# Kernel optimization log

Hardware: AMD Instinct MI355X
Metric: run time of the kernel (lower is better)

The kernel has to match this reference:

```python
import jax, jax.numpy as jnp
import numpy as np

B, S1, S2, S3, I, O = 4, 64, 64, 64, 32, 32
MX, MZ = 16, 16
HID = O * 2  # factor=2 feedforward hidden


def setup_inputs() -> dict:
    key = jax.random.key(0)
    ks = jax.random.split(key, 5)
    x = jax.random.normal(ks[0], (B, S1, S2, S3, I), jnp.float32)
    # xavier-normal-ish scale for complex fourier weights stored as [...,2]
    sw = np.float32(np.sqrt(2.0 / (I + O)))
    wx = jax.random.normal(ks[1], (I, O, MX, 2), jnp.float32) * sw
    wz = jax.random.normal(ks[2], (I, O, MZ, 2), jnp.float32) * sw
    w1 = jax.random.normal(ks[3], (O, HID), jnp.float32) * np.float32(np.sqrt(1.0 / O))
    b1 = jnp.zeros((HID,), jnp.float32)
    w2 = jax.random.normal(ks[4], (HID, O), jnp.float32) * np.float32(np.sqrt(1.0 / HID))
    b2 = jnp.zeros((O,), jnp.float32)
    return {"x": x, "wx": wx, "wz": wz, "w1": w1, "b1": b1, "w2": w2, "b2": b2}


def _forward_fourier(x, wx, wz):
    # x: [b, i, s1, s2, s3]
    # z-axis branch
    cwz = wz[..., 0] + 1j * wz[..., 1]          # [i, o, mz] complex
    xfz = jnp.fft.rfft(x, axis=-1, norm='ortho')  # [b,i,s1,s2,S3//2+1]
    pz = jnp.einsum('bixyz,ioz->boxyz', xfz[..., :MZ], cwz)
    pz = jnp.pad(pz, ((0, 0), (0, 0), (0, 0), (0, 0), (0, S3 // 2 + 1 - MZ)))
    xz = jnp.fft.irfft(pz, n=S3, axis=-1, norm='ortho')
    # x-axis branch (note: modes_y branch contributes 0 in the source, xy=0.0)
    cwx = wx[..., 0] + 1j * wx[..., 1]          # [i, o, mx]
    xfx = jnp.fft.rfft(x, axis=2, norm='ortho')  # [b,i,S1//2+1,s2,s3]
    px = jnp.einsum('bixyz,iox->boxyz', xfx[:, :, :MX], cwx)
    px = jnp.pad(px, ((0, 0), (0, 0), (0, S1 // 2 + 1 - MX), (0, 0), (0, 0)))
    xx = jnp.fft.irfft(px, n=S1, axis=2, norm='ortho')
    return xx + xz


def reference(x, wx, wz, w1, b1, w2, b2):
    xt = jnp.transpose(x, (0, 4, 1, 2, 3))      # b i s1 s2 s3
    y = _forward_fourier(xt, wx, wz)
    y = jnp.transpose(y, (0, 2, 3, 4, 1))       # b s1 s2 s3 o
    # backcast FeedForward: Linear -> ReLU -> Linear (dropout=0, no norms)
    h = jax.nn.relu(y @ w1 + b1)
    b_out = h @ w2 + b2
    return b_out
```

## Files before the change

kernel.cpp:

```cpp
#include <hip/hip_runtime.h>

namespace {

typedef _Float16 half_t;
typedef half_t f16x2 __attribute__((ext_vector_type(2)));
typedef half_t f16x8 __attribute__((ext_vector_type(8)));
typedef float f32x4 __attribute__((ext_vector_type(4)));

constexpr size_t RSTR = 64 * 64 * 32;

constexpr int WS_TF = 0;
constexpr int WS_TI = 2048;
constexpr int WS_WZ = 4096;
constexpr int WS_WX = 69632;
constexpr int WS_W1 = 135168;
constexpr int WS_W2 = 137216;

__device__ __forceinline__ float f4get(const float4& v, int u) {
  return u == 0 ? v.x : (u == 1 ? v.y : (u == 2 ? v.z : v.w));
}

__device__ __forceinline__ f32x4 mfma16(f16x8 a, f16x8 b, f32x4 c) {
  return __builtin_amdgcn_mfma_f32_16x16x32_f16(a, b, c, 0, 0, 0);
}

__global__ __launch_bounds__(256) void kinit(const float* __restrict__ wx,
                                             const float* __restrict__ wz,
                                             const float* __restrict__ w1,
                                             const float* __restrict__ w2,
                                             half_t* __restrict__ wsh) {
  const int id = blockIdx.x * 256 + threadIdx.x;
  const int l = id & 63, r = l & 15, g = l >> 4;
  f16x8 frag;
  if (id < 256) {
    int fid = id >> 6, mt = fid >> 1, kt = fid & 1;
#pragma unroll
    for (int e = 0; e < 8; ++e) {
      int k = kt * 32 + 8 * g + e;
      int mc = mt * 16 + r, m = mc >> 1, p = mc & 1;
      float s, c;
      sincospif((float)(m * k) * (1.0f / 32.0f), &s, &c);
      frag[e] = (half_t)(0.125f * (p ? -s : c));
    }
    *(f16x8*)(wsh + WS_TF + (size_t)id * 8) = frag;
  } else if (id < 512) {
    int id2 = id - 256, mt = id2 >> 6;
#pragma unroll
    for (int e = 0; e < 8; ++e) {
      int zp = mt * 16 + r;
      int k = 8 * g + e, m = k >> 1, p = k & 1;
      float s, c;
      sincospif((float)(m * zp) * (1.0f / 32.0f), &s, &c);
      float sc = (m == 0) ? 0.125f : 0.25f;
      frag[e] = (half_t)(p ? -sc * s : sc * c);
    }
    *(f16x8*)(wsh + WS_TI + (size_t)id2 * 8) = frag;
  } else if (id < 16896) {
    int id2 = id - 512;
    const float* wsrc = wz;
    size_t off = WS_WZ;
    if (id2 >= 8192) { id2 -= 8192; wsrc = wx; off = WS_WX; }
    int fid = id2 >> 6, m = fid >> 3, kt = (fid >> 2) & 1, nt = fid & 3;
#pragma unroll
    for (int e = 0; e < 8; ++e) {
      int k = kt * 32 + 8 * g + e, i = k >> 1, p = k & 1;
      int n = nt * 16 + r, o = n >> 1, q = n & 1;
      int base = ((i * 32 + o) * 16 + m) * 2;
      float re = wsrc[base], im = wsrc[base + 1];
      frag[e] = (half_t)(q ? (p ? re : im) : (p ? -im : re));
    }
    *(f16x8*)(wsh + off + (size_t)id2 * 8) = frag;
  } else if (id < 17152) {
    int id2 = id - 16896, nt = id2 >> 6;
#pragma unroll
    for (int e = 0; e < 8; ++e) {
      int k = 8 * g + e, n = nt * 16 + r;
      frag[e] = (half_t)w1[k * 64 + n];
    }
    *(f16x8*)(wsh + WS_W1 + (size_t)id2 * 8) = frag;
  } else if (id < 17408) {
    int id2 = id - 17152, fid = id2 >> 6, kt = fid >> 1, nt = fid & 1;
#pragma unroll
    for (int e = 0; e < 8; ++e) {
      int k = kt * 32 + 8 * g + e, n = nt * 16 + r;
      frag[e] = (half_t)w2[k * 32 + n];
    }
    *(f16x8*)(wsh + WS_W2 + (size_t)id2 * 8) = frag;
  }
}

template <int BR>
__global__ __launch_bounds__(256) void kspec(const float* __restrict__ x,
                                             const half_t* __restrict__ wsh,
                                             const float* __restrict__ b1g,
                                             const float* __restrict__ b2g,
                                             float* __restrict__ outf) {
  __shared__ __align__(16) char smraw[49152];
  half_t* XB = (half_t*)smraw;
  half_t* FB = (half_t*)smraw;
  half_t* PB = (half_t*)(smraw + 32768);
  half_t* outh = (half_t*)outf;
  const int t = threadIdx.x, l = t & 63, w = t >> 6, r = l & 15, g = l >> 4;
  const f32x4 vzero = {0.f, 0.f, 0.f, 0.f};

  const int col0 = blockIdx.x * 8;
  size_t xbase = (size_t)col0 * 2048, zstr = 32, cstr = 2048;

  {
    int c = t >> 5, sub = t & 31;
    int i4 = (sub & 7) * 4, zq = sub >> 3;
    const float* xp = x + xbase + (size_t)c * cstr + i4;
#pragma unroll
    for (int zo = 0; zo < 2; ++zo) {
      int zb = zq * 16 + zo * 8;
      float4 v[8];
#pragma unroll
      for (int zz = 0; zz < 8; ++zz)
        v[zz] = *(const float4*)(xp + (size_t)(zb + zz) * zstr);
#pragma unroll
      for (int u = 0; u < 4; ++u) {
        f16x8 rowv;
#pragma unroll
        for (int zz = 0; zz < 8; ++zz) rowv[zz] = (half_t)f4get(v[zz], u);
        int rowi = c * 32 + i4 + u;
        int gr = (zb >> 3) ^ (rowi & 7);
        *(f16x8*)(XB + rowi * 64 + gr * 8) = rowv;
      }
    }
  }
  __syncthreads();

  f32x4 fa[2][4];
#pragma unroll
  for (int mt = 0; mt < 2; ++mt)
#pragma unroll
    for (int nt = 0; nt < 4; ++nt) fa[mt][nt] = vzero;
  {
    f16x8 Atf[2][2], Bx[4][2];
#pragma unroll
    for (int mt = 0; mt < 2; ++mt)
#pragma unroll
      for (int kt = 0; kt < 2; ++kt)
        Atf[mt][kt] = *(const f16x8*)(wsh + WS_TF + (size_t)((mt * 2 + kt) * 64 + l) * 8);
#pragma unroll
    for (int nt = 0; nt < 4; ++nt)
#pragma unroll
      for (int kt = 0; kt < 2; ++kt) {
        int rowi = w * 64 + nt * 16 + r;
        int gr = (kt * 4 + g) ^ (rowi & 7);
        Bx[nt][kt] = *(const f16x8*)(XB + rowi * 64 + gr * 8);
      }
#pragma unroll
    for (int kt = 0; kt < 2; ++kt)
#pragma unroll
      for (int nt = 0; nt < 4; ++nt)
#pragma unroll
        for (int mt = 0; mt < 2; ++mt)
          fa[mt][nt] = mfma16(Atf[mt][kt], Bx[nt][kt], fa[mt][nt]);
  }
  __syncthreads();

#pragma unroll
  for (int mt = 0; mt < 2; ++mt)
#pragma unroll
    for (int nt = 0; nt < 4; ++nt)
#pragma unroll
      for (int q = 0; q < 4; ++q) {
        int mc = mt * 16 + 4 * g + q, m = mc >> 1, p = mc & 1;
        int n = w * 64 + nt * 16 + r, c = n >> 5, i = n & 31;
        int k = 2 * i + p;
        FB[(m * 16 + c) * 64 + ((k >> 3) ^ (c & 7)) * 8 + (k & 7)] = (half_t)fa[mt][nt][q];
      }
  __syncthreads();

  const half_t* WF = wsh + WS_WZ;
#pragma unroll
  for (int j = 0; j < 4; ++j) {
    int m = w * 4 + j;
    f16x8 Af[2];
#pragma unroll
    for (int kt = 0; kt < 2; ++kt) {
      int gr = (kt * 4 + g) ^ (r & 7);
      Af[kt] = *(const f16x8*)(FB + (m * 16 + r) * 64 + gr * 8);
    }
    f32x4 pa[4];
#pragma unroll
    for (int nt = 0; nt < 4; ++nt) pa[nt] = vzero;
#pragma unroll
    for (int kt = 0; kt < 2; ++kt)
#pragma unroll
      for (int nt = 0; nt < 4; ++nt) {
        f16x8 Bw = *(const f16x8*)(WF + (size_t)((m * 8 + kt * 4 + nt) * 64 + l) * 8);
        pa[nt] = mfma16(Af[kt], Bw, pa[nt]);
      }
#pragma unroll
    for (int nt = 0; nt < 4; ++nt)
#pragma unroll
      for (int q = 0; q < 4; ++q) {
        int c = 4 * g + q;
        if (c < 8) {
          int n = nt * 16 + r, o = n >> 1, q2 = n & 1;
          int k = 2 * m + q2;
          PB[(c * 32 + o) * 32 + ((k >> 3) ^ (o & 3)) * 8 + (k & 7)] = (half_t)pa[nt][q];
        }
      }
  }
  __syncthreads();

  {
    f16x8 Ati[4];
#pragma unroll
    for (int mt = 0; mt < 4; ++mt)
      Ati[mt] = *(const f16x8*)(wsh + WS_TI + (size_t)(mt * 64 + l) * 8);
#pragma unroll
    for (int cc = 0; cc < 2; ++cc) {
      int c = w * 2 + cc;
      f16x8 Bp[2];
#pragma unroll
      for (int nt = 0; nt < 2; ++nt) {
        int o = nt * 16 + r;
        Bp[nt] = *(const f16x8*)(PB + (c * 32 + o) * 32 + (g ^ (o & 3)) * 8);
      }
      f32x4 ya[4][2];
#pragma unroll
      for (int mt = 0; mt < 4; ++mt)
#pragma unroll
        for (int nt = 0; nt < 2; ++nt) ya[mt][nt] = mfma16(Ati[mt], Bp[nt], vzero);
#pragma unroll
      for (int mt = 0; mt < 4; ++mt)
#pragma unroll
        for (int nt = 0; nt < 2; ++nt)
#pragma unroll
          for (int q = 0; q < 4; ++q) {
            int zp = mt * 16 + 4 * g + q, o = nt * 16 + r;
            outh[(size_t)(col0 + c) * 4096 + zp * 64 + o] = (half_t)ya[mt][nt][q];
          }
    }
  }
}

__global__ __launch_bounds__(256, 4) void kx4(const float* __restrict__ x,
                                              const half_t* __restrict__ wsh,
                                              const float* __restrict__ b1g,
                                              const float* __restrict__ b2g,
                                              float* __restrict__ outf) {
  __shared__ __align__(16) half_t smh[16384];
  half_t* XB = smh;
  half_t* FB = smh + 8192;
  half_t* PB = smh + 12288;
  half_t* YL = smh;
  half_t* HLa = smh + 8192;
  half_t* HLb = smh + 12288;
  half_t* outh = (half_t*)outf;
  const int t = threadIdx.x, l = t & 63, w = t >> 6, r = l & 15, g = l >> 4;
  const f32x4 vzero = {0.f, 0.f, 0.f, 0.f};

  const int d = blockIdx.x;
  const int pp = (d & 7) * 512 + (d >> 3);
  const int col0 = pp * 4;
  const int b = col0 >> 12, s2 = (col0 >> 6) & 63, s30 = col0 & 63;
  const size_t xbase = (size_t)b * 8388608 + (size_t)s2 * 2048 + (size_t)s30 * 32;

  {
    int sub = t & 31, zq = t >> 5;
    int c = sub >> 3, i4 = (sub & 7) * 4;
    const float* xp = x + xbase + (size_t)c * 32 + i4 + (size_t)(zq * 8) * RSTR;
    float4 v[8];
#pragma unroll
    for (int zz = 0; zz < 8; ++zz) v[zz] = *(const float4*)(xp + (size_t)zz * RSTR);
#pragma unroll
    for (int u = 0; u < 4; ++u) {
      f16x8 rowv;
#pragma unroll
      for (int zz = 0; zz < 8; ++zz) rowv[zz] = (half_t)f4get(v[zz], u);
      int rowi = c * 32 + i4 + u;
      int key = (rowi ^ (rowi >> 2)) & 7;
      *(f16x8*)(XB + rowi * 64 + (zq ^ key) * 8) = rowv;
    }
  }
  __syncthreads();

  f32x4 fa[2][2];
  {
    f16x8 Atf[2][2], Bx[2][2];
#pragma unroll
    for (int mt = 0; mt < 2; ++mt)
#pragma unroll
      for (int kt = 0; kt < 2; ++kt)
        Atf[mt][kt] = *(const f16x8*)(wsh + WS_TF + (size_t)((mt * 2 + kt) * 64 + l) * 8);
#pragma unroll
    for (int nt = 0; nt < 2; ++nt)
#pragma unroll
      for (int kt = 0; kt < 2; ++kt) {
        int rowi = w * 32 + nt * 16 + r;
        int key = (rowi ^ (rowi >> 2)) & 7;
        Bx[nt][kt] = *(const f16x8*)(XB + rowi * 64 + (((kt * 4 + g) ^ key)) * 8);
      }
#pragma unroll
    for (int mt = 0; mt < 2; ++mt)
#pragma unroll
      for (int nt = 0; nt < 2; ++nt) fa[mt][nt] = vzero;
#pragma unroll
    for (int kt = 0; kt < 2; ++kt)
#pragma unroll
      for (int nt = 0; nt < 2; ++nt)
#pragma unroll
        for (int mt = 0; mt < 2; ++mt)
          fa[mt][nt] = mfma16(Atf[mt][kt], Bx[nt][kt], fa[mt][nt]);
  }
#pragma unroll
  for (int mt = 0; mt < 2; ++mt)
#pragma unroll
    for (int nt = 0; nt < 2; ++nt)
#pragma unroll
      for (int pr = 0; pr < 2; ++pr) {
        int q = 2 * pr;
        int mc = mt * 16 + 4 * g + q, m = mc >> 1;
        int n = w * 32 + nt * 16 + r, c = n >> 5, i = n & 31;
        int k = 2 * i;
        f16x2 pairv = {(half_t)fa[mt][nt][q], (half_t)fa[mt][nt][q + 1]};
        *(f16x2*)(FB + (m * 4 + c) * 64 + (((k >> 3) ^ ((m + 2 * c) & 7))) * 8 + (k & 7)) =
            pairv;
      }
  __syncthreads();

#pragma unroll
  for (int j = 0; j < 4; ++j) {
    int m = w * 4 + j;
    int rsel = r & 3, keym = (m + 2 * rsel) & 7;
    f16x8 Af[2];
#pragma unroll
    for (int kt = 0; kt < 2; ++kt)
      Af[kt] = *(const f16x8*)(FB + (m * 4 + rsel) * 64 + (((kt * 4 + g) ^ keym)) * 8);
    f32x4 pa[4];
#pragma unroll
    for (int nt = 0; nt < 4; ++nt) pa[nt] = vzero;
#pragma unroll
    for (int kt = 0; kt < 2; ++kt)
#pragma unroll
      for (int nt = 0; nt < 4; ++nt) {
        f16x8 Bw = *(const f16x8*)(wsh + WS_WX + (size_t)((m * 8 + kt * 4 + nt) * 64 + l) * 8);
        pa[nt] = mfma16(Af[kt], Bw, pa[nt]);
      }
    if (g == 0) {
#pragma unroll
      for (int nt = 0; nt < 4; ++nt)
#pragma unroll
        for (int q = 0; q < 4; ++q) {
          int c = q;
          int n = nt * 16 + r, o = n >> 1, q2 = n & 1;
          int k = 2 * m + q2;
          PB[(c * 32 + o) * 32 + (((k >> 3) ^ (o & 3))) * 8 + (k & 7)] = (half_t)pa[nt][q];
        }
    }
  }
  __syncthreads();

  f16x8 Bp[2];
#pragma unroll
  for (int nt = 0; nt < 2; ++nt) {
    int o = nt * 16 + r;
    Bp[nt] = *(const f16x8*)(PB + (w * 32 + o) * 32 + ((g ^ (o & 3))) * 8);
  }
  f16x8 Ati[4];
#pragma unroll
  for (int mt = 0; mt < 4; ++mt)
    Ati[mt] = *(const f16x8*)(wsh + WS_TI + (size_t)(mt * 64 + l) * 8);
  f16x8 yzf[4];
#pragma unroll
  for (int rr = 0; rr < 4; ++rr) {
    int zp = rr * 16 + r;
    yzf[rr] = *(const f16x8*)(outh + ((size_t)(b * 64 + zp) * 64 + s2) * 4096 +
                              (size_t)(s30 + w) * 64 + 8 * g);
  }
  f16x8 W1F[4];
#pragma unroll
  for (int nt = 0; nt < 4; ++nt)
    W1F[nt] = *(const f16x8*)(wsh + WS_W1 + (size_t)(nt * 64 + l) * 8);
  float b1v[4];
#pragma unroll
  for (int nt = 0; nt < 4; ++nt) b1v[nt] = b1g[nt * 16 + r];

  half_t* YLw = YL + w * 2048;
  {
    f32x4 ya[4][2];
#pragma unroll
    for (int mt = 0; mt < 4; ++mt)
#pragma unroll
      for (int nt = 0; nt < 2; ++nt) ya[mt][nt] = mfma16(Ati[mt], Bp[nt], vzero);
#pragma unroll
    for (int mt = 0; mt < 4; ++mt)
#pragma unroll
      for (int nt = 0; nt < 2; ++nt)
#pragma unroll
        for (int q = 0; q < 4; ++q) {
          int zp = mt * 16 + 4 * g + q, o = nt * 16 + r;
          YLw[zp * 32 + (((o >> 3) ^ ((zp >> 2) & 3))) * 8 + (o & 7)] = (half_t)ya[mt][nt][q];
        }
  }
  f16x8 W2F[4];
#pragma unroll
  for (int f = 0; f < 4; ++f)
    W2F[f] = *(const f16x8*)(wsh + WS_W2 + (size_t)(f * 64 + l) * 8);
  float b2v[2];
#pragma unroll
  for (int nt = 0; nt < 2; ++nt) b2v[nt] = b2g[nt * 16 + r];

  half_t* HLwa = HLa + w * 1024;
  half_t* HLwb = HLb + w * 1024;
#pragma unroll
  for (int rr = 0; rr < 4; ++rr) {
    half_t* HLw = (rr & 1) ? HLwb : HLwa;
    int rowl = rr * 16 + r;
    f16x8 AY = *(const f16x8*)(YLw + rowl * 32 + ((g ^ ((rowl >> 2) & 3))) * 8);
    AY = AY + yzf[rr];
    f32x4 ha[4];
#pragma unroll
    for (int nt = 0; nt < 4; ++nt) ha[nt] = mfma16(AY, W1F[nt], vzero);
#pragma unroll
    for (int nt = 0; nt < 4; ++nt)
#pragma unroll
      for (int q = 0; q < 4; ++q) {
        int row4 = 4 * g + q, n = nt * 16 + r;
        float hv = fmaxf(ha[nt][q] + b1v[nt], 0.f);
        HLw[row4 * 64 + (((n >> 3) ^ g)) * 8 + (n & 7)] = (half_t)hv;
      }
    f16x8 AH[2];
#pragma unroll
    for (int kt = 0; kt < 2; ++kt)
      AH[kt] = *(const f16x8*)(HLw + r * 64 + (((kt * 4 + g) ^ (r >> 2))) * 8);
    f32x4 oa[2];
#pragma unroll
    for (int nt = 0; nt < 2; ++nt) oa[nt] = vzero;
#pragma unroll
    for (int kt = 0; kt < 2; ++kt)
#pragma unroll
      for (int nt = 0; nt < 2; ++nt) oa[nt] = mfma16(AH[kt], W2F[kt * 2 + nt], oa[nt]);
#pragma unroll
    for (int nt = 0; nt < 2; ++nt)
#pragma unroll
      for (int q = 0; q < 4; ++q) {
        int zp = rr * 16 + 4 * g + q, o = nt * 16 + r;
        outf[(size_t)b * 8388608 + (size_t)zp * RSTR + (size_t)s2 * 2048 +
             (size_t)(s30 + w) * 32 + o] = oa[nt][q] + b2v[nt];
      }
  }
}

}

extern "C" void kernel_launch(void* const* d_in, const int* in_sizes, int n_in,
                              void* d_out, int out_size, void* d_ws, size_t ws_size,
                              hipStream_t stream) {
  const float* x = (const float*)d_in[0];
  const float* wx = (const float*)d_in[1];
  const float* wz = (const float*)d_in[2];
  const float* w1 = (const float*)d_in[3];
  const float* b1 = (const float*)d_in[4];
  const float* w2 = (const float*)d_in[5];
  const float* b2 = (const float*)d_in[6];
  float* out = (float*)d_out;
  half_t* wsh = (half_t*)d_ws;

  hipLaunchKernelGGL(kinit, dim3(68), dim3(256), 0, stream, wx, wz, w1, w2, wsh);
  hipLaunchKernelGGL((kspec<0>), dim3(2048), dim3(256), 0, stream, x, wsh, b1, b2, out);
  hipLaunchKernelGGL(kx4, dim3(4096), dim3(256), 0, stream, x, wsh, b1, b2, out);
}
```

Baseline: 134.8 us.

## Load x fragments directly into registers and remap FFN rows across waves

Result: slower. 138.0 us (+2.4%).

```diff
diff --git a/kernel.cpp b/kernel.cpp
--- a/kernel.cpp
+++ b/kernel.cpp
@@ -244,13 +244,11 @@
                                               const float* __restrict__ b1g,
                                               const float* __restrict__ b2g,
                                               float* __restrict__ outf) {
-  __shared__ __align__(16) half_t smh[16384];
-  half_t* XB = smh;
-  half_t* FB = smh + 8192;
-  half_t* PB = smh + 12288;
+  __shared__ __align__(16) half_t smh[12288];
+  half_t* FB = smh;
+  half_t* PB = smh + 4096;
   half_t* YL = smh;
-  half_t* HLa = smh + 8192;
-  half_t* HLb = smh + 12288;
+  half_t* HL = smh + 8192;
   half_t* outh = (half_t*)outf;
   const int t = threadIdx.x, l = t & 63, w = t >> 6, r = l & 15, g = l >> 4;
   const f32x4 vzero = {0.f, 0.f, 0.f, 0.f};
@@ -261,41 +259,26 @@
   const int b = col0 >> 12, s2 = (col0 >> 6) & 63, s30 = col0 & 63;
   const size_t xbase = (size_t)b * 8388608 + (size_t)s2 * 2048 + (size_t)s30 * 32;
 
-  {
-    int sub = t & 31, zq = t >> 5;
-    int c = sub >> 3, i4 = (sub & 7) * 4;
-    const float* xp = x + xbase + (size_t)c * 32 + i4 + (size_t)(zq * 8) * RSTR;
-    float4 v[8];
-#pragma unroll
-    for (int zz = 0; zz < 8; ++zz) v[zz] = *(const float4*)(xp + (size_t)zz * RSTR);
-#pragma unroll
-    for (int u = 0; u < 4; ++u) {
-      f16x8 rowv;
-#pragma unroll
-      for (int zz = 0; zz < 8; ++zz) rowv[zz] = (half_t)f4get(v[zz], u);
-      int rowi = c * 32 + i4 + u;
-      int key = (rowi ^ (rowi >> 2)) & 7;
-      *(f16x8*)(XB + rowi * 64 + (zq ^ key) * 8) = rowv;
-    }
-  }
-  __syncthreads();
-
   f32x4 fa[2][2];
   {
-    f16x8 Atf[2][2], Bx[2][2];
+    f16x8 Bx[2][2];
+    const float* bp = x + xbase + (size_t)w * 32 + r;
+#pragma unroll
+    for (int nt = 0; nt < 2; ++nt)
+#pragma unroll
+      for (int kt = 0; kt < 2; ++kt) {
+        f16x8 fr;
+#pragma unroll
+        for (int e = 0; e < 8; ++e)
+          fr[e] = (half_t)bp[(size_t)(nt * 16) + (size_t)(kt * 32 + 8 * g + e) * RSTR];
+        Bx[nt][kt] = fr;
+      }
+    f16x8 Atf[2][2];
 #pragma unroll
     for (int mt = 0; mt < 2; ++mt)
 #pragma unroll
       for (int kt = 0; kt < 2; ++kt)
         Atf[mt][kt] = *(const f16x8*)(wsh + WS_TF + (size_t)((mt * 2 + kt) * 64 + l) * 8);
-#pragma unroll
-    for (int nt = 0; nt < 2; ++nt)
-#pragma unroll
-      for (int kt = 0; kt < 2; ++kt) {
-        int rowi = w * 32 + nt * 16 + r;
-        int key = (rowi ^ (rowi >> 2)) & 7;
-        Bx[nt][kt] = *(const f16x8*)(XB + rowi * 64 + (((kt * 4 + g) ^ key)) * 8);
-      }
 #pragma unroll
     for (int mt = 0; mt < 2; ++mt)
 #pragma unroll
@@ -362,6 +345,8 @@
     int o = nt * 16 + r;
     Bp[nt] = *(const f16x8*)(PB + (w * 32 + o) * 32 + ((g ^ (o & 3))) * 8);
   }
+  __syncthreads();
+
   f16x8 Ati[4];
 #pragma unroll
   for (int mt = 0; mt < 4; ++mt)
@@ -369,9 +354,8 @@
   f16x8 yzf[4];
 #pragma unroll
   for (int rr = 0; rr < 4; ++rr) {
-    int zp = rr * 16 + r;
-    yzf[rr] = *(const f16x8*)(outh + ((size_t)(b * 64 + zp) * 64 + s2) * 4096 +
-                              (size_t)(s30 + w) * 64 + 8 * g);
+    yzf[rr] = *(const f16x8*)(outh + ((size_t)(b * 64 + w * 16 + r) * 64 + s2) * 4096 +
+                              (size_t)(s30 + rr) * 64 + 8 * g);
   }
   f16x8 W1F[4];
 #pragma unroll
@@ -380,8 +364,6 @@
   float b1v[4];
 #pragma unroll
   for (int nt = 0; nt < 4; ++nt) b1v[nt] = b1g[nt * 16 + r];
-
-  half_t* YLw = YL + w * 2048;
   {
     f32x4 ya[4][2];
 #pragma unroll
@@ -395,9 +377,13 @@
 #pragma unroll
         for (int q = 0; q < 4; ++q) {
           int zp = mt * 16 + 4 * g + q, o = nt * 16 + r;
-          YLw[zp * 32 + (((o >> 3) ^ ((zp >> 2) & 3))) * 8 + (o & 7)] = (half_t)ya[mt][nt][q];
+          int rowi = w * 64 + zp;
+          YL[rowi * 32 + (((o >> 3) ^ ((rowi >> 2) & 3))) * 8 + (o & 7)] =
+              (half_t)ya[mt][nt][q];
         }
   }
+  __syncthreads();
+
   f16x8 W2F[4];
 #pragma unroll
   for (int f = 0; f < 4; ++f)
@@ -406,13 +392,10 @@
 #pragma unroll
   for (int nt = 0; nt < 2; ++nt) b2v[nt] = b2g[nt * 16 + r];
 
-  half_t* HLwa = HLa + w * 1024;
-  half_t* HLwb = HLb + w * 1024;
 #pragma unroll
   for (int rr = 0; rr < 4; ++rr) {
-    half_t* HLw = (rr & 1) ? HLwb : HLwa;
-    int rowl = rr * 16 + r;
-    f16x8 AY = *(const f16x8*)(YLw + rowl * 32 + ((g ^ ((rowl >> 2) & 3))) * 8);
+    int rowA = rr * 64 + w * 16 + r;
+    f16x8 AY = *(const f16x8*)(YL + rowA * 32 + ((g ^ ((rowA >> 2) & 3))) * 8);
     AY = AY + yzf[rr];
     f32x4 ha[4];
 #pragma unroll
@@ -421,14 +404,16 @@
     for (int nt = 0; nt < 4; ++nt)
 #pragma unroll
       for (int q = 0; q < 4; ++q) {
-        int row4 = 4 * g + q, n = nt * 16 + r;
+        int rloc = w * 16 + 4 * g + q, n = nt * 16 + r;
         float hv = fmaxf(ha[nt][q] + b1v[nt], 0.f);
-        HLw[row4 * 64 + (((n >> 3) ^ g)) * 8 + (n & 7)] = (half_t)hv;
-      }
+        HL[rloc * 64 + (((n >> 3) ^ ((rloc >> 2) & 7))) * 8 + (n & 7)] = (half_t)hv;
+      }
+    __syncthreads();
+    int rA2 = w * 16 + r;
     f16x8 AH[2];
 #pragma unroll
     for (int kt = 0; kt < 2; ++kt)
-      AH[kt] = *(const f16x8*)(HLw + r * 64 + (((kt * 4 + g) ^ (r >> 2))) * 8);
+      AH[kt] = *(const f16x8*)(HL + rA2 * 64 + (((kt * 4 + g) ^ ((rA2 >> 2) & 7))) * 8);
     f32x4 oa[2];
 #pragma unroll
     for (int nt = 0; nt < 2; ++nt) oa[nt] = vzero;
@@ -440,10 +425,11 @@
     for (int nt = 0; nt < 2; ++nt)
 #pragma unroll
       for (int q = 0; q < 4; ++q) {
-        int zp = rr * 16 + 4 * g + q, o = nt * 16 + r;
+        int zp = w * 16 + 4 * g + q, o = nt * 16 + r;
         outf[(size_t)b * 8388608 + (size_t)zp * RSTR + (size_t)s2 * 2048 +
-             (size_t)(s30 + w) * 32 + o] = oa[nt][q] + b2v[nt];
-      }
+             (size_t)(s30 + rr) * 32 + o] = oa[nt][q] + b2v[nt];
+      }
+    if (rr < 3) __syncthreads();
   }
 }
 
```
